# Performance work log

Hardware: AMD Instinct MI355X
Metric: run time of the kernel (lower is better)

## Reference

```python
import jax, jax.numpy as jnp
import numpy as np

X_DIM, H_DIM, Y_DIM, ROLLOUT = 256, 2048, 256, 4096


def setup_inputs() -> dict:
    key = jax.random.key(0)
    ks = jax.random.split(key, 6)
    inp = {
        "x": jax.random.normal(ks[0], (1, ROLLOUT, X_DIM), dtype=jnp.float32),
        "h": jnp.zeros((H_DIM,), dtype=jnp.float32),
        "Wc": jax.random.normal(ks[1], (X_DIM + H_DIM, H_DIM), dtype=jnp.float32) * 0.01,
        "Wu": jax.random.normal(ks[2], (X_DIM + H_DIM, H_DIM), dtype=jnp.float32) * 0.01,
        "Wr": jax.random.normal(ks[3], (X_DIM + H_DIM, H_DIM), dtype=jnp.float32) * 0.01,
        "bc": jnp.zeros((H_DIM,), dtype=jnp.float32),
        "bu": jnp.zeros((H_DIM,), dtype=jnp.float32),
        "br": jnp.zeros((H_DIM,), dtype=jnp.float32),
        "Wh_y": jax.random.normal(ks[4], (H_DIM, Y_DIM), dtype=jnp.float32) * 0.01,
        "by": jnp.zeros((Y_DIM,), dtype=jnp.float32),
    }
    return inp


def reference(x, h, Wc, Wu, Wr, bc, bu, br, Wh_y, by):
    xs = x[0]  # [T, x_dim]

    def step(hid, xt):
        xc = jnp.concatenate([xt, hid])                      # [x_dim + h_dim]
        Lu = jax.nn.sigmoid(xc @ Wu + bu)                    # update gate
        Lr = jax.nn.sigmoid(xc @ Wr + br)                    # reset gate
        xr = jnp.concatenate([xt, hid * Lr])
        c_tilda = jnp.tanh(xr @ Wc + bc)
        h_new = c_tilda * Lu + hid * (1.0 - Lu)
        y = h_new @ Wh_y + by
        return h_new, y

    h_fin, ys = jax.lax.scan(step, h, xs)  # ys: [T, y_dim]
    return ys, h_fin
```

## Files before the change

kernel.cpp:

```cpp
#include <hip/hip_runtime.h>
#include <hip/hip_bf16.h>

#define TSTEPS 4096
#define XD 256
#define HD 2048
#define YD 256
#define KD 2304
#define NWG 256
#define NT 512

#define WU_OFF 0
#define WR_OFF (8*KD*2)
#define WC_OFF (16*KD*2)
#define WY_OFF (24*KD*2)
#define HBUF_OFF (WY_OFF + HD*4)
#define ZBUF_OFF (HBUF_OFF + HD*4)
#define RED_OFF (ZBUF_OFF + HD*4)
#define LDS_BYTES (RED_OFF + 256)

#define HGO_U32 0
#define RGO_U32 256
#define WS_ZERO_BYTES 34816
#define HB0_OFF 2048
#define HB1_OFF 10240
#define RB0_OFF 18432
#define RB1_OFF 26624

__device__ __forceinline__ float bflo(unsigned u){ return __uint_as_float(u << 16); }
__device__ __forceinline__ float bfhi(unsigned u){ return __uint_as_float(u & 0xffff0000u); }
__device__ __forceinline__ unsigned short f2bf(float f){
  unsigned b = __float_as_uint(f);
  b += 0x7fffu + ((b >> 16) & 1u);
  return (unsigned short)(b >> 16);
}
__device__ __forceinline__ float sigmoidf_(float x){ return 1.0f / (1.0f + __expf(-x)); }

__device__ __forceinline__ void storetag(float* p, float v, unsigned tag){
  unsigned b = (__float_as_uint(v) & ~3u) | tag;
  __hip_atomic_store((unsigned*)p, b, __ATOMIC_RELAXED, __HIP_MEMORY_SCOPE_AGENT);
}
__device__ __forceinline__ void flagst(unsigned* p, unsigned v){
  __hip_atomic_store(p, v, __ATOMIC_RELAXED, __HIP_MEMORY_SCOPE_AGENT);
}
__device__ __forceinline__ void spinflag(const unsigned* p, unsigned epoch, long* budget){
  while (__hip_atomic_load(p, __ATOMIC_RELAXED, __HIP_MEMORY_SCOPE_AGENT) < epoch) {
    if (--(*budget) < 0) break;
    __builtin_amdgcn_s_sleep(1);
  }
}

__device__ __forceinline__ float4 pollchunk16(const float4* p, unsigned tag, long* budget){
  for (;;) {
    float4 r;
    asm volatile("global_load_dwordx4 %0, %1, off sc1\n\t"
                 "s_waitcnt vmcnt(0)"
                 : "=v"(r) : "v"(p) : "memory");
    unsigned m = (__float_as_uint(r.x)^tag) | (__float_as_uint(r.y)^tag)
               | (__float_as_uint(r.z)^tag) | (__float_as_uint(r.w)^tag);
    if ((m & 3u) == 0u) return r;
    if (--(*budget) < 0) return r;
    __builtin_amdgcn_s_sleep(1);
  }
}

__device__ __forceinline__ float4 cohload16(const float4* p){
  float4 r;
  asm volatile("global_load_dwordx4 %0, %1, off sc1\n\t"
               "s_waitcnt vmcnt(0)"
               : "=v"(r) : "v"(p) : "memory");
  return r;
}

template<int I0, int I1, int STRIDE>
__device__ __forceinline__ void dotacc(const float* v, const unsigned short* wcol,
                                       int lane, float4& acc){
  #pragma unroll
  for (int i = I0; i < I1; ++i) {
    int k = 4 * (lane + STRIDE * i);
    float4 vv = *(const float4*)(v + k);
    uint2  wq = *(const uint2*)(wcol + k);
    acc.x = fmaf(vv.x, bflo(wq.x), acc.x);
    acc.y = fmaf(vv.y, bfhi(wq.x), acc.y);
    acc.z = fmaf(vv.z, bflo(wq.y), acc.z);
    acc.w = fmaf(vv.w, bfhi(wq.y), acc.w);
  }
}
__device__ __forceinline__ void xpart(const float4 xq, const unsigned short* wcol,
                                      int l6, float4& acc){
  uint2 wq = *(const uint2*)(wcol + 4*l6);
  acc.x = fmaf(xq.x, bflo(wq.x), acc.x);
  acc.y = fmaf(xq.y, bfhi(wq.x), acc.y);
  acc.z = fmaf(xq.z, bflo(wq.y), acc.z);
  acc.w = fmaf(xq.w, bfhi(wq.y), acc.w);
}
__device__ __forceinline__ float redux64(float4 a){
  float s = (a.x + a.y) + (a.z + a.w);
  s += __shfl_xor(s, 32); s += __shfl_xor(s, 16); s += __shfl_xor(s, 8);
  s += __shfl_xor(s, 4);  s += __shfl_xor(s, 2);  s += __shfl_xor(s, 1);
  return s;
}

extern "C" __global__ void __launch_bounds__(NT)
gru_persistent(const float* __restrict__ x,  const float* __restrict__ h0,
               const float* __restrict__ Wc, const float* __restrict__ Wu,
               const float* __restrict__ Wr, const float* __restrict__ bc,
               const float* __restrict__ bu, const float* __restrict__ br,
               const float* __restrict__ Wy, const float* __restrict__ by,
               float* __restrict__ out, unsigned* wsu)
{
  extern __shared__ char smem[];
  unsigned short* wuS = (unsigned short*)(smem + WU_OFF);
  unsigned short* wrS = (unsigned short*)(smem + WR_OFF);
  unsigned short* wcS = (unsigned short*)(smem + WC_OFF);
  float* wyS   = (float*)(smem + WY_OFF);
  float* hbufS = (float*)(smem + HBUF_OFF);
  float* zbufS = (float*)(smem + ZBUF_OFF);
  float* red   = (float*)(smem + RED_OFF);

  unsigned* hgo = wsu + HGO_U32;
  unsigned* rgo = wsu + RGO_U32;
  float* hb[2] = { (float*)((char*)wsu + HB0_OFF), (float*)((char*)wsu + HB1_OFF) };
  float* rb[2] = { (float*)((char*)wsu + RB0_OFF), (float*)((char*)wsu + RB1_OFF) };

  const int wg = blockIdx.x, tid = threadIdx.x;
  const int col0 = 8 * wg;

  for (int idx = tid; idx < 8*KD; idx += NT) {
    int c = idx & 7, k = idx >> 3;
    size_t g = (size_t)k * HD + col0 + c;
    wuS[c*KD + k] = f2bf(Wu[g]);
    wrS[c*KD + k] = f2bf(Wr[g]);
    wcS[c*KD + k] = f2bf(Wc[g]);
  }
  for (int k = tid; k < HD; k += NT) wyS[k] = Wy[(size_t)k * YD + wg];
  if (tid < 8) {
    red[16+tid] = bu[col0+tid];
    red[24+tid] = br[col0+tid];
    red[32+tid] = bc[col0+tid];
    red[56+tid] = h0[col0+tid];
  }
  if (tid == 0) red[40] = by[wg];
  __syncthreads();

  long budget = 20000000;

  const int w  = tid >> 6, l6 = tid & 63;
  const unsigned short* ucol = wuS + w * KD;
  const unsigned short* rcol = wrS + w * KD;
  const unsigned short* ccol = wcS + w * KD;

  float4 xq = ((const float4*)x)[l6];
  float ureg = 0.f;

  auto window = [&](int t){
    float4 au = make_float4(0.f, 0.f, 0.f, 0.f);
    xpart(xq, ucol, l6, au);
    dotacc<1, 9, 64>(hbufS - XD, ucol, l6, au);
    ureg = sigmoidf_(redux64(au) + red[16 + w]);
    int k = 256 * w + 4 * l6;
    float4 hv4 = *(const float4*)(hbufS + k);
    float4 wy4 = *(const float4*)(wyS + k);
    float ys = fmaf(hv4.x, wy4.x, fmaf(hv4.y, wy4.y, fmaf(hv4.z, wy4.z, hv4.w * wy4.w)));
    ys += __shfl_xor(ys, 32); ys += __shfl_xor(ys, 16); ys += __shfl_xor(ys, 8);
    ys += __shfl_xor(ys, 4);  ys += __shfl_xor(ys, 2);  ys += __shfl_xor(ys, 1);
    if (l6 == 0) red[8 + w] = ys;
    if (t + 1 < TSTEPS) xq = ((const float4*)(x + (size_t)(t+1) * XD))[l6];
  };

  for (int t = 0; t < TSTEPS; ++t) {
    float4 a1 = make_float4(0.f, 0.f, 0.f, 0.f);
    xpart(xq, rcol, l6, a1);

    if (t == 0) {
      ((float4*)hbufS)[tid] = ((const float4*)h0)[tid];
    } else if (wg == 0) {
      float4 hv = pollchunk16((const float4*)hb[(t+1)&1] + tid,
                              (unsigned)(t & 3), &budget);
      __syncthreads();
      if (tid < 8) flagst(hgo + tid*32, (unsigned)t);
      ((float4*)hbufS)[tid] = hv;
    } else {
      if (tid == 0) spinflag(hgo + (wg & 7)*32, (unsigned)t, &budget);
      __syncthreads();
      ((float4*)hbufS)[tid] = cohload16((const float4*)hb[(t+1)&1] + tid);
    }
    __syncthreads();

    dotacc<1, 9, 64>(hbufS - XD, rcol, l6, a1);
    {
      float s = redux64(a1);
      if (l6 == 0)
        storetag(rb[t&1] + col0 + w,
                 sigmoidf_(s + red[24 + w]) * red[56 + w],
                 (unsigned)((t+1) & 3));
    }

    float4 a2 = make_float4(0.f, 0.f, 0.f, 0.f);
    xpart(xq, ccol, l6, a2);

    if (wg == 0) {
      float4 zv = pollchunk16((const float4*)rb[t&1] + tid,
                              (unsigned)((t+1) & 3), &budget);
      __syncthreads();
      if (tid < 8) flagst(rgo + tid*32, (unsigned)(t+1));
      ((float4*)zbufS)[tid] = zv;
      window(t);
    } else {
      window(t);
      if (tid == 0) spinflag(rgo + (wg & 7)*32, (unsigned)(t+1), &budget);
      __syncthreads();
      ((float4*)zbufS)[tid] = cohload16((const float4*)rb[t&1] + tid);
    }
    __syncthreads();

    if (tid == 0 && t > 0) {
      float y = red[8]+red[9]+red[10]+red[11]+red[12]+red[13]+red[14]+red[15] + red[40];
      out[(size_t)(t-1) * YD + wg] = y;
    }

    dotacc<1, 9, 64>(zbufS - XD, ccol, l6, a2);
    {
      float s = redux64(a2);
      if (l6 == 0) {
        float cc = tanhf(s + red[32 + w]);
        float hp = red[56 + w];
        float hn = cc * ureg + hp * (1.0f - ureg);
        red[56 + w] = hn;
        storetag(hb[t&1] + col0 + w, hn, (unsigned)((t+1) & 3));
      }
    }
  }

  if (wg == 0) {
    float4 hv = pollchunk16((const float4*)hb[(TSTEPS-1)&1] + tid,
                            (unsigned)(TSTEPS & 3), &budget);
    __syncthreads();
    if (tid < 8) flagst(hgo + tid*32, (unsigned)TSTEPS);
    ((float4*)hbufS)[tid] = hv;
  } else {
    if (tid == 0) spinflag(hgo + (wg & 7)*32, (unsigned)TSTEPS, &budget);
    __syncthreads();
    ((float4*)hbufS)[tid] = cohload16((const float4*)hb[(TSTEPS-1)&1] + tid);
  }
  __syncthreads();
  {
    int k = 256 * w + 4 * l6;
    float4 hv4 = *(const float4*)(hbufS + k);
    float4 wy4 = *(const float4*)(wyS + k);
    float ys = fmaf(hv4.x, wy4.x, fmaf(hv4.y, wy4.y, fmaf(hv4.z, wy4.z, hv4.w * wy4.w)));
    ys += __shfl_xor(ys, 32); ys += __shfl_xor(ys, 16); ys += __shfl_xor(ys, 8);
    ys += __shfl_xor(ys, 4);  ys += __shfl_xor(ys, 2);  ys += __shfl_xor(ys, 1);
    if (l6 == 0) red[8 + w] = ys;
  }
  __syncthreads();
  if (tid == 0) {
    float y = red[8]+red[9]+red[10]+red[11]+red[12]+red[13]+red[14]+red[15] + red[40];
    out[(size_t)(TSTEPS-1) * YD + wg] = y;
  }
  if (tid < 8) out[(size_t)TSTEPS * YD + col0 + tid] = red[56 + tid];
}

extern "C" void kernel_launch(void* const* d_in, const int* in_sizes, int n_in,
                              void* d_out, int out_size, void* d_ws, size_t ws_size,
                              hipStream_t stream) {
  const float* x  = (const float*)d_in[0];
  const float* h0 = (const float*)d_in[1];
  const float* Wc = (const float*)d_in[2];
  const float* Wu = (const float*)d_in[3];
  const float* Wr = (const float*)d_in[4];
  const float* bc = (const float*)d_in[5];
  const float* bu = (const float*)d_in[6];
  const float* br = (const float*)d_in[7];
  const float* Wy = (const float*)d_in[8];
  const float* by = (const float*)d_in[9];
  float* out = (float*)d_out;
  unsigned* wsu = (unsigned*)d_ws;

  (void)hipFuncSetAttribute((const void*)gru_persistent,
                            hipFuncAttributeMaxDynamicSharedMemorySize, LDS_BYTES);
  (void)hipMemsetAsync(d_ws, 0, WS_ZERO_BYTES, stream);
  gru_persistent<<<dim3(NWG), dim3(NT), LDS_BYTES, stream>>>(
      x, h0, Wc, Wu, Wr, bc, bu, br, Wy, by, out, wsu);
}
```

Measured before the change: 23.07 ms.

## Pad per-workgroup exchange slots to cache lines and fan out go-flags per wave

Each workgroup now writes its slice of the hidden and reset-gated vectors into its own 128-byte line instead of packing them contiguously. The master workgroup polls each line with two loads per thread. The go-flags are spread across 64 lines, with each wave spinning on its own flag rather than one thread per workgroup, which removes a barrier before the coherent reload. This aims to cut false sharing and contention on the global exchange buffers and to shorten the per-step barrier chain. In exchange it uses a larger zeroed workspace and more flag stores per step.

```diff
diff --git a/kernel.cpp b/kernel.cpp
--- a/kernel.cpp
+++ b/kernel.cpp
@@ -19,12 +19,13 @@
 #define LDS_BYTES (RED_OFF + 256)
 
 #define HGO_U32 0
-#define RGO_U32 256
-#define WS_ZERO_BYTES 34816
-#define HB0_OFF 2048
-#define HB1_OFF 10240
-#define RB0_OFF 18432
-#define RB1_OFF 26624
+#define RGO_U32 2048
+#define HB0_OFF 16384
+#define HB1_OFF 49152
+#define RB0_OFF 81920
+#define RB1_OFF 114688
+#define WS_ZERO_BYTES 147456
+#define LSTRIDE 32
 
 __device__ __forceinline__ float bflo(unsigned u){ return __uint_as_float(u << 16); }
 __device__ __forceinline__ float bfhi(unsigned u){ return __uint_as_float(u & 0xffff0000u); }
@@ -49,16 +50,19 @@
   }
 }
 
-__device__ __forceinline__ float4 pollchunk16(const float4* p, unsigned tag, long* budget){
+__device__ __forceinline__ void polline32(const float4* p, unsigned tag, long* budget,
+                                          float4& r0, float4& r1){
   for (;;) {
-    float4 r;
-    asm volatile("global_load_dwordx4 %0, %1, off sc1\n\t"
+    asm volatile("global_load_dwordx4 %0, %2, off sc1\n\t"
+                 "global_load_dwordx4 %1, %2, off offset:16 sc1\n\t"
                  "s_waitcnt vmcnt(0)"
-                 : "=v"(r) : "v"(p) : "memory");
-    unsigned m = (__float_as_uint(r.x)^tag) | (__float_as_uint(r.y)^tag)
-               | (__float_as_uint(r.z)^tag) | (__float_as_uint(r.w)^tag);
-    if ((m & 3u) == 0u) return r;
-    if (--(*budget) < 0) return r;
+                 : "=v"(r0), "=v"(r1) : "v"(p) : "memory");
+    unsigned m = (__float_as_uint(r0.x)^tag) | (__float_as_uint(r0.y)^tag)
+               | (__float_as_uint(r0.z)^tag) | (__float_as_uint(r0.w)^tag)
+               | (__float_as_uint(r1.x)^tag) | (__float_as_uint(r1.y)^tag)
+               | (__float_as_uint(r1.z)^tag) | (__float_as_uint(r1.w)^tag);
+    if ((m & 3u) == 0u) return;
+    if (--(*budget) < 0) return;
     __builtin_amdgcn_s_sleep(1);
   }
 }
@@ -145,6 +149,9 @@
   long budget = 20000000;
 
   const int w  = tid >> 6, l6 = tid & 63;
+  const int goline = ((wg & 7) << 3) + w;
+  const int sw = tid >> 1, half = tid & 1;
+  const int gidx = sw * (LSTRIDE/4) + half;
   const unsigned short* ucol = wuS + w * KD;
   const unsigned short* rcol = wrS + w * KD;
   const unsigned short* ccol = wcS + w * KD;
@@ -173,24 +180,29 @@
 
     if (t == 0) {
       ((float4*)hbufS)[tid] = ((const float4*)h0)[tid];
+      __syncthreads();
     } else if (wg == 0) {
-      float4 hv = pollchunk16((const float4*)hb[(t+1)&1] + tid,
-                              (unsigned)(t & 3), &budget);
-      __syncthreads();
-      if (tid < 8) flagst(hgo + tid*32, (unsigned)t);
+      if (tid < NWG) {
+        float4 r0, r1;
+        polline32((const float4*)hb[(t+1)&1] + tid*(LSTRIDE/4),
+                  (unsigned)(t & 3), &budget, r0, r1);
+        ((float4*)hbufS)[2*tid]   = r0;
+        ((float4*)hbufS)[2*tid+1] = r1;
+      }
+      __syncthreads();
+      if (tid < 64) flagst(hgo + tid*32, (unsigned)t);
+    } else {
+      if (l6 == 0) spinflag(hgo + goline*32, (unsigned)t, &budget);
+      float4 hv = cohload16((const float4*)hb[(t+1)&1] + gidx);
       ((float4*)hbufS)[tid] = hv;
-    } else {
-      if (tid == 0) spinflag(hgo + (wg & 7)*32, (unsigned)t, &budget);
-      __syncthreads();
-      ((float4*)hbufS)[tid] = cohload16((const float4*)hb[(t+1)&1] + tid);
-    }
-    __syncthreads();
+      __syncthreads();
+    }
 
     dotacc<1, 9, 64>(hbufS - XD, rcol, l6, a1);
     {
       float s = redux64(a1);
       if (l6 == 0)
-        storetag(rb[t&1] + col0 + w,
+        storetag(rb[t&1] + wg*LSTRIDE + w,
                  sigmoidf_(s + red[24 + w]) * red[56 + w],
                  (unsigned)((t+1) & 3));
     }
@@ -199,19 +211,24 @@
     xpart(xq, ccol, l6, a2);
 
     if (wg == 0) {
-      float4 zv = pollchunk16((const float4*)rb[t&1] + tid,
-                              (unsigned)((t+1) & 3), &budget);
-      __syncthreads();
-      if (tid < 8) flagst(rgo + tid*32, (unsigned)(t+1));
-      ((float4*)zbufS)[tid] = zv;
+      if (tid < NWG) {
+        float4 r0, r1;
+        polline32((const float4*)rb[t&1] + tid*(LSTRIDE/4),
+                  (unsigned)((t+1) & 3), &budget, r0, r1);
+        ((float4*)zbufS)[2*tid]   = r0;
+        ((float4*)zbufS)[2*tid+1] = r1;
+      }
+      __syncthreads();
+      if (tid < 64) flagst(rgo + tid*32, (unsigned)(t+1));
       window(t);
+      __syncthreads();
     } else {
       window(t);
-      if (tid == 0) spinflag(rgo + (wg & 7)*32, (unsigned)(t+1), &budget);
-      __syncthreads();
-      ((float4*)zbufS)[tid] = cohload16((const float4*)rb[t&1] + tid);
-    }
-    __syncthreads();
+      if (l6 == 0) spinflag(rgo + goline*32, (unsigned)(t+1), &budget);
+      float4 rv = cohload16((const float4*)rb[t&1] + gidx);
+      ((float4*)zbufS)[tid] = rv;
+      __syncthreads();
+    }
 
     if (tid == 0 && t > 0) {
       float y = red[8]+red[9]+red[10]+red[11]+red[12]+red[13]+red[14]+red[15] + red[40];
@@ -226,23 +243,28 @@
         float hp = red[56 + w];
         float hn = cc * ureg + hp * (1.0f - ureg);
         red[56 + w] = hn;
-        storetag(hb[t&1] + col0 + w, hn, (unsigned)((t+1) & 3));
+        storetag(hb[t&1] + wg*LSTRIDE + w, hn,
+                 (unsigned)((t+1) & 3));
       }
     }
   }
 
   if (wg == 0) {
-    float4 hv = pollchunk16((const float4*)hb[(TSTEPS-1)&1] + tid,
-                            (unsigned)(TSTEPS & 3), &budget);
+    if (tid < NWG) {
+      float4 r0, r1;
+      polline32((const float4*)hb[(TSTEPS-1)&1] + tid*(LSTRIDE/4),
+                (unsigned)(TSTEPS & 3), &budget, r0, r1);
+      ((float4*)hbufS)[2*tid]   = r0;
+      ((float4*)hbufS)[2*tid+1] = r1;
+    }
     __syncthreads();
-    if (tid < 8) flagst(hgo + tid*32, (unsigned)TSTEPS);
+    if (tid < 64) flagst(hgo + tid*32, (unsigned)TSTEPS);
+  } else {
+    if (l6 == 0) spinflag(hgo + goline*32, (unsigned)TSTEPS, &budget);
+    float4 hv = cohload16((const float4*)hb[(TSTEPS-1)&1] + gidx);
     ((float4*)hbufS)[tid] = hv;
-  } else {
-    if (tid == 0) spinflag(hgo + (wg & 7)*32, (unsigned)TSTEPS, &budget);
     __syncthreads();
-    ((float4*)hbufS)[tid] = cohload16((const float4*)hb[(TSTEPS-1)&1] + tid);
-  }
-  __syncthreads();
+  }
   {
     int k = 256 * w + 4 * l6;
     float4 hv4 = *(const float4*)(hbufS + k);
```

Measured after the change: 24.29 ms. 1.05x slower.

## Pad per-workgroup exchange lines and republish gathered state to dense buffers

Applied to the files above, without the earlier changes.

Each workgroup now writes its 8 hidden/reset values into a private 128-byte-strided line, which removes false sharing between producers. Workgroup 0 gathers these lines and republishes them as a dense buffer that other workgroups read. Each wave now spins on its own go-flag (64 flags instead of 8), which drops one workgroup barrier per exchange and spreads polling traffic across cache lines. The cost is an extra store pass by the aggregator, more flag stores, and a larger workspace.

```diff
diff --git a/kernel.cpp b/kernel.cpp
--- a/kernel.cpp
+++ b/kernel.cpp
@@ -19,12 +19,17 @@
 #define LDS_BYTES (RED_OFF + 256)
 
 #define HGO_U32 0
-#define RGO_U32 256
-#define WS_ZERO_BYTES 34816
-#define HB0_OFF 2048
-#define HB1_OFF 10240
-#define RB0_OFF 18432
-#define RB1_OFF 26624
+#define ZGO_U32 2048
+#define HP0_OFF 16384
+#define HP1_OFF 49152
+#define ZP0_OFF 81920
+#define ZP1_OFF 114688
+#define HD0_OFF 147456
+#define HD1_OFF 155648
+#define ZD0_OFF 163840
+#define ZD1_OFF 172032
+#define WS_ZERO_BYTES 180224
+#define LSTRIDE 32
 
 __device__ __forceinline__ float bflo(unsigned u){ return __uint_as_float(u << 16); }
 __device__ __forceinline__ float bfhi(unsigned u){ return __uint_as_float(u & 0xffff0000u); }
@@ -48,7 +53,6 @@
     __builtin_amdgcn_s_sleep(1);
   }
 }
-
 __device__ __forceinline__ float4 pollchunk16(const float4* p, unsigned tag, long* budget){
   for (;;) {
     float4 r;
@@ -62,13 +66,19 @@
     __builtin_amdgcn_s_sleep(1);
   }
 }
-
 __device__ __forceinline__ float4 cohload16(const float4* p){
   float4 r;
   asm volatile("global_load_dwordx4 %0, %1, off sc1\n\t"
                "s_waitcnt vmcnt(0)"
                : "=v"(r) : "v"(p) : "memory");
   return r;
+}
+__device__ __forceinline__ void stchunk16(float* p, float4 v){
+  unsigned* q = (unsigned*)p;
+  __hip_atomic_store(q+0, __float_as_uint(v.x), __ATOMIC_RELAXED, __HIP_MEMORY_SCOPE_AGENT);
+  __hip_atomic_store(q+1, __float_as_uint(v.y), __ATOMIC_RELAXED, __HIP_MEMORY_SCOPE_AGENT);
+  __hip_atomic_store(q+2, __float_as_uint(v.z), __ATOMIC_RELAXED, __HIP_MEMORY_SCOPE_AGENT);
+  __hip_atomic_store(q+3, __float_as_uint(v.w), __ATOMIC_RELAXED, __HIP_MEMORY_SCOPE_AGENT);
 }
 
 template<int I0, int I1, int STRIDE>
@@ -118,9 +128,11 @@
   float* red   = (float*)(smem + RED_OFF);
 
   unsigned* hgo = wsu + HGO_U32;
-  unsigned* rgo = wsu + RGO_U32;
-  float* hb[2] = { (float*)((char*)wsu + HB0_OFF), (float*)((char*)wsu + HB1_OFF) };
-  float* rb[2] = { (float*)((char*)wsu + RB0_OFF), (float*)((char*)wsu + RB1_OFF) };
+  unsigned* zgo = wsu + ZGO_U32;
+  float* hp[2]  = { (float*)((char*)wsu + HP0_OFF), (float*)((char*)wsu + HP1_OFF) };
+  float* zp[2]  = { (float*)((char*)wsu + ZP0_OFF), (float*)((char*)wsu + ZP1_OFF) };
+  float* hdg[2] = { (float*)((char*)wsu + HD0_OFF), (float*)((char*)wsu + HD1_OFF) };
+  float* zdg[2] = { (float*)((char*)wsu + ZD0_OFF), (float*)((char*)wsu + ZD1_OFF) };
 
   const int wg = blockIdx.x, tid = threadIdx.x;
   const int col0 = 8 * wg;
@@ -145,6 +157,8 @@
   long budget = 20000000;
 
   const int w  = tid >> 6, l6 = tid & 63;
+  const int goline = ((wg & 7) << 3) + w;
+  const int pline = tid >> 1, pchk = tid & 1;
   const unsigned short* ucol = wuS + w * KD;
   const unsigned short* rcol = wrS + w * KD;
   const unsigned short* ccol = wcS + w * KD;
@@ -173,24 +187,26 @@
 
     if (t == 0) {
       ((float4*)hbufS)[tid] = ((const float4*)h0)[tid];
+      __syncthreads();
     } else if (wg == 0) {
-      float4 hv = pollchunk16((const float4*)hb[(t+1)&1] + tid,
+      float4 hv = pollchunk16((const float4*)(hp[(t+1)&1] + pline*LSTRIDE + pchk*4),
                               (unsigned)(t & 3), &budget);
-      __syncthreads();
-      if (tid < 8) flagst(hgo + tid*32, (unsigned)t);
+      stchunk16(hdg[(t+1)&1] + 4*tid, hv);
       ((float4*)hbufS)[tid] = hv;
+      __syncthreads();
+      if (tid < 64) flagst(hgo + tid*32, (unsigned)t);
     } else {
-      if (tid == 0) spinflag(hgo + (wg & 7)*32, (unsigned)t, &budget);
-      __syncthreads();
-      ((float4*)hbufS)[tid] = cohload16((const float4*)hb[(t+1)&1] + tid);
-    }
-    __syncthreads();
+      if (l6 == 0) spinflag(hgo + goline*32, (unsigned)t, &budget);
+      float4 hv = cohload16((const float4*)hdg[(t+1)&1] + tid);
+      ((float4*)hbufS)[tid] = hv;
+      __syncthreads();
+    }
 
     dotacc<1, 9, 64>(hbufS - XD, rcol, l6, a1);
     {
       float s = redux64(a1);
       if (l6 == 0)
-        storetag(rb[t&1] + col0 + w,
+        storetag(zp[t&1] + wg*LSTRIDE + w,
                  sigmoidf_(s + red[24 + w]) * red[56 + w],
                  (unsigned)((t+1) & 3));
     }
@@ -199,19 +215,21 @@
     xpart(xq, ccol, l6, a2);
 
     if (wg == 0) {
-      float4 zv = pollchunk16((const float4*)rb[t&1] + tid,
+      float4 zv = pollchunk16((const float4*)(zp[t&1] + pline*LSTRIDE + pchk*4),
                               (unsigned)((t+1) & 3), &budget);
-      __syncthreads();
-      if (tid < 8) flagst(rgo + tid*32, (unsigned)(t+1));
+      stchunk16(zdg[t&1] + 4*tid, zv);
       ((float4*)zbufS)[tid] = zv;
+      __syncthreads();
+      if (tid < 64) flagst(zgo + tid*32, (unsigned)(t+1));
       window(t);
+      __syncthreads();
     } else {
       window(t);
-      if (tid == 0) spinflag(rgo + (wg & 7)*32, (unsigned)(t+1), &budget);
-      __syncthreads();
-      ((float4*)zbufS)[tid] = cohload16((const float4*)rb[t&1] + tid);
-    }
-    __syncthreads();
+      if (l6 == 0) spinflag(zgo + goline*32, (unsigned)(t+1), &budget);
+      float4 zv = cohload16((const float4*)zdg[t&1] + tid);
+      ((float4*)zbufS)[tid] = zv;
+      __syncthreads();
+    }
 
     if (tid == 0 && t > 0) {
       float y = red[8]+red[9]+red[10]+red[11]+red[12]+red[13]+red[14]+red[15] + red[40];
@@ -223,26 +241,28 @@
       float s = redux64(a2);
       if (l6 == 0) {
         float cc = tanhf(s + red[32 + w]);
-        float hp = red[56 + w];
-        float hn = cc * ureg + hp * (1.0f - ureg);
+        float hp_ = red[56 + w];
+        float hn = cc * ureg + hp_ * (1.0f - ureg);
         red[56 + w] = hn;
-        storetag(hb[t&1] + col0 + w, hn, (unsigned)((t+1) & 3));
+        storetag(hp[t&1] + wg*LSTRIDE + w, hn,
+                 (unsigned)((t+1) & 3));
       }
     }
   }
 
   if (wg == 0) {
-    float4 hv = pollchunk16((const float4*)hb[(TSTEPS-1)&1] + tid,
+    float4 hv = pollchunk16((const float4*)(hp[(TSTEPS+1)&1] + pline*LSTRIDE + pchk*4),
                             (unsigned)(TSTEPS & 3), &budget);
+    stchunk16(hdg[(TSTEPS+1)&1] + 4*tid, hv);
+    ((float4*)hbufS)[tid] = hv;
     __syncthreads();
-    if (tid < 8) flagst(hgo + tid*32, (unsigned)TSTEPS);
+    if (tid < 64) flagst(hgo + tid*32, (unsigned)TSTEPS);
+  } else {
+    if (l6 == 0) spinflag(hgo + goline*32, (unsigned)TSTEPS, &budget);
+    float4 hv = cohload16((const float4*)hdg[(TSTEPS+1)&1] + tid);
     ((float4*)hbufS)[tid] = hv;
-  } else {
-    if (tid == 0) spinflag(hgo + (wg & 7)*32, (unsigned)TSTEPS, &budget);
     __syncthreads();
-    ((float4*)hbufS)[tid] = cohload16((const float4*)hb[(TSTEPS-1)&1] + tid);
-  }
-  __syncthreads();
+  }
   {
     int k = 256 * w + 4 * l6;
     float4 hv4 = *(const float4*)(hbufS + k);
```

Measured after the change: 24.83 ms. 1.08x slower.
